# Optimization experiments

Hardware: AMD Instinct MI355X
Metric: run time of the kernel (lower is better)

Reference implementation:

```python
import jax, jax.numpy as jnp
import numpy as np

B, T, S, D, K = 512, 49, 200, 512, 128


def setup_inputs() -> dict:
    key = jax.random.key(0)
    ks = jax.random.split(key, 8)
    return {
        "ifeature": jax.random.normal(ks[0], (B, T, D), dtype=jnp.float32),
        "tfeature_h": jax.random.normal(ks[1], (B, S, D), dtype=jnp.float32),
        "w_Dense_Vi_0": jax.random.normal(ks[2], (D, K), dtype=jnp.float32) * 0.05,
        "w_Dense_Vt_0": jax.random.normal(ks[3], (D, K), dtype=jnp.float32) * 0.05,
        "w_Dense_Pi_0": jax.random.normal(ks[4], (2 * K, 1), dtype=jnp.float32) * 0.05,
        "b_Dense_Pi_0": jnp.zeros((T,), dtype=jnp.float32),
        "w_Dense_Vi_1": jax.random.normal(ks[5], (D, K), dtype=jnp.float32) * 0.05,
        "w_Dense_Vt_1": jax.random.normal(ks[6], (D, K), dtype=jnp.float32) * 0.05,
        "w_Dense_Pi_1": jax.random.normal(ks[7], (2 * K, 1), dtype=jnp.float32) * 0.05,
        "b_Dense_Pi_1": jnp.zeros((S,), dtype=jnp.float32),
    }


def reference(ifeature, tfeature_h, w_Dense_Vi_0, w_Dense_Vt_0, w_Dense_Pi_0,
              b_Dense_Pi_0, w_Dense_Vi_1, w_Dense_Vt_1, w_Dense_Pi_1, b_Dense_Pi_1):
    # tfeature: mean-pooled text, [B, D]
    tfeature = jnp.mean(tfeature_h, axis=1)

    # --- attention over image regions (title_len) ---
    w_Vi_0 = jnp.einsum('btd,dk->btk', ifeature, w_Dense_Vi_0)          # [B,T,K]
    w_Vt_0 = (tfeature @ w_Dense_Vt_0)[:, None, :]                      # [B,1,K] broadcast to T
    Hi = jnp.tanh(jnp.concatenate(
        [w_Vi_0, jnp.broadcast_to(w_Vt_0, w_Vi_0.shape)], axis=-1))     # [B,T,2K]
    Hi_w_b = jnp.einsum('btk,k->bt', Hi, w_Dense_Pi_0[:, 0]) + b_Dense_Pi_0
    Pi = jax.nn.softmax(Hi_w_b, axis=-1)                                # [B,T]
    Vi = jnp.einsum('bt,btd->bd', Pi, ifeature)                         # attended image feature

    # --- attention over text tokens (seq_len) ---
    w_Vi_1 = (Vi @ w_Dense_Vi_1)[:, None, :]                            # [B,1,K]
    w_Vt_1 = jnp.einsum('bsd,dk->bsk', tfeature_h, w_Dense_Vt_1)        # [B,S,K]
    Ht = jnp.tanh(jnp.concatenate(
        [jnp.broadcast_to(w_Vi_1, w_Vt_1.shape), w_Vt_1], axis=-1))     # [B,S,2K]
    Ht_b = jnp.einsum('bsk,k->bs', Ht, w_Dense_Pi_1[:, 0]) + b_Dense_Pi_1
    Pt = jax.nn.softmax(Ht_b, axis=-1)                                  # [B,S]

    # NOTE: original call() returns Pt_Vt (weighted tokens), not the pooled Vt.
    Pt_Vt = Pt[:, :, None] * tfeature_h                                 # [B,S,D]
    return Pt_Vt
```

## Files before the change

### kernel.cpp

```cpp
#include <hip/hip_runtime.h>
#include <math.h>

#define BB 512
#define SS 200
#define DD 512
#define KK 128

typedef __attribute__((ext_vector_type(8))) short bf16x8;
typedef __attribute__((ext_vector_type(4))) float f32x4;

__device__ inline unsigned short f2bf(float f) {
    union { float f; unsigned int u; } v; v.f = f;
    unsigned int r = v.u + 0x7FFFu + ((v.u >> 16) & 1u);
    return (unsigned short)(r >> 16);
}

__global__ void wt_kernel(const float* __restrict__ W, unsigned short* __restrict__ Wt) {
    int i = blockIdx.x * 256 + threadIdx.x;
    int col = i >> 9, d = i & 511;
    Wt[i] = f2bf(W[d * KK + col]);
}

__global__ __launch_bounds__(512, 4) void fused_kernel(
    const float* __restrict__ tfh,
    const unsigned short* __restrict__ Wt,
    const float* __restrict__ wpk,
    const float* __restrict__ bias,
    float* __restrict__ out)
{
    __shared__ unsigned short As[256][40];
    __shared__ unsigned short Bs[128][40];
    __shared__ float logit_s[256];
    __shared__ float Pt[SS];
    __shared__ float wpart[8];

    int tid = threadIdx.x;
    int w   = tid >> 6;
    int l   = tid & 63;
    int l15 = l & 15;
    int g   = l >> 4;
    int b   = blockIdx.x;
    const float* Ab = tfh + (size_t)b * SS * DD;

    f32x4 acc[2][8];
    #pragma unroll
    for (int m = 0; m < 2; ++m)
        #pragma unroll
        for (int n = 0; n < 8; ++n) acc[m][n] = (f32x4){0.f, 0.f, 0.f, 0.f};

    float wv[8];
    #pragma unroll
    for (int n = 0; n < 8; ++n) wv[n] = wpk[n * 16 + l15];

    int ar  = tid >> 1;
    int arc = (ar < SS) ? ar : (SS - 1);
    int ac  = (tid & 1) * 16;
    const float* aptr = Ab + (size_t)arc * DD + ac;
    const unsigned short* bptr = Wt + (size_t)(tid >> 1) * DD + ac;

    for (int d0 = 0; d0 < DD; d0 += 32) {
        {
            const float* s_ = aptr + d0;
            float4 v0 = *(const float4*)(s_);
            float4 v1 = *(const float4*)(s_ + 4);
            float4 v2 = *(const float4*)(s_ + 8);
            float4 v3 = *(const float4*)(s_ + 12);
            bf16x8 p0, p1;
            p0[0] = (short)f2bf(v0.x); p0[1] = (short)f2bf(v0.y);
            p0[2] = (short)f2bf(v0.z); p0[3] = (short)f2bf(v0.w);
            p0[4] = (short)f2bf(v1.x); p0[5] = (short)f2bf(v1.y);
            p0[6] = (short)f2bf(v1.z); p0[7] = (short)f2bf(v1.w);
            p1[0] = (short)f2bf(v2.x); p1[1] = (short)f2bf(v2.y);
            p1[2] = (short)f2bf(v2.z); p1[3] = (short)f2bf(v2.w);
            p1[4] = (short)f2bf(v3.x); p1[5] = (short)f2bf(v3.y);
            p1[6] = (short)f2bf(v3.z); p1[7] = (short)f2bf(v3.w);
            *(bf16x8*)&As[ar][ac]     = p0;
            *(bf16x8*)&As[ar][ac + 8] = p1;
        }
        if (tid < 256) {
            bf16x8 q0 = *(const bf16x8*)(bptr + d0);
            bf16x8 q1 = *(const bf16x8*)(bptr + d0 + 8);
            *(bf16x8*)&Bs[tid >> 1][ac]     = q0;
            *(bf16x8*)&Bs[tid >> 1][ac + 8] = q1;
        }
        __syncthreads();
        bf16x8 af0 = *(const bf16x8*)&As[w * 32 + l15][g * 8];
        bf16x8 af1 = *(const bf16x8*)&As[w * 32 + 16 + l15][g * 8];
        #pragma unroll
        for (int n = 0; n < 8; ++n) {
            bf16x8 bf = *(const bf16x8*)&Bs[n * 16 + l15][g * 8];
            acc[0][n] = __builtin_amdgcn_mfma_f32_16x16x32_bf16(af0, bf, acc[0][n], 0, 0, 0);
            acc[1][n] = __builtin_amdgcn_mfma_f32_16x16x32_bf16(af1, bf, acc[1][n], 0, 0, 0);
        }
        __syncthreads();
    }

    float rs[2][4];
    #pragma unroll
    for (int m = 0; m < 2; ++m)
        #pragma unroll
        for (int r = 0; r < 4; ++r) rs[m][r] = 0.f;
    #pragma unroll
    for (int m = 0; m < 2; ++m)
        #pragma unroll
        for (int n = 0; n < 8; ++n)
            #pragma unroll
            for (int r = 0; r < 4; ++r)
                rs[m][r] += tanhf(acc[m][n][r]) * wv[n];
    #pragma unroll
    for (int m = 0; m < 2; ++m)
        #pragma unroll
        for (int r = 0; r < 4; ++r) {
            float v = rs[m][r];
            v += __shfl_xor(v, 1, 64);
            v += __shfl_xor(v, 2, 64);
            v += __shfl_xor(v, 4, 64);
            v += __shfl_xor(v, 8, 64);
            rs[m][r] = v;
        }
    if (l15 == 0) {
        #pragma unroll
        for (int m = 0; m < 2; ++m)
            #pragma unroll
            for (int r = 0; r < 4; ++r) {
                int srow = w * 32 + m * 16 + g * 4 + r;
                if (srow < SS) logit_s[srow] = rs[m][r] + bias[srow];
            }
    }
    __syncthreads();

    float v = (tid < SS) ? logit_s[tid] : -INFINITY;
    float m = v;
    #pragma unroll
    for (int off = 32; off > 0; off >>= 1) m = fmaxf(m, __shfl_xor(m, off, 64));
    if (l == 0) wpart[w] = m;
    __syncthreads();
    m = -INFINITY;
    #pragma unroll
    for (int i = 0; i < 8; ++i) m = fmaxf(m, wpart[i]);
    float e = (tid < SS) ? expf(v - m) : 0.f;
    float ssum = e;
    #pragma unroll
    for (int off = 32; off > 0; off >>= 1) ssum += __shfl_xor(ssum, off, 64);
    __syncthreads();
    if (l == 0) wpart[w] = ssum;
    __syncthreads();
    ssum = 0.f;
    #pragma unroll
    for (int i = 0; i < 8; ++i) ssum += wpart[i];
    if (tid < SS) Pt[tid] = e / ssum;
    __syncthreads();

    const float4* src = (const float4*)Ab;
    float4*       dst = (float4*)(out + (size_t)b * SS * DD);
    const int n4 = SS * DD / 4;
    for (int i = tid; i < n4; i += 512) {
        float p = Pt[i >> 7];
        float4 x = src[i];
        x.x *= p; x.y *= p; x.z *= p; x.w *= p;
        dst[i] = x;
    }
}

extern "C" void kernel_launch(void* const* d_in, const int* in_sizes, int n_in,
                              void* d_out, int out_size, void* d_ws, size_t ws_size,
                              hipStream_t stream) {
    const float* tfh   = (const float*)d_in[1];
    const float* wVt1  = (const float*)d_in[7];
    const float* wp1   = (const float*)d_in[8];
    const float* bias1 = (const float*)d_in[9];
    float* out = (float*)d_out;

    unsigned short* Wt = (unsigned short*)d_ws;

    wt_kernel<<<KK * DD / 256, 256, 0, stream>>>(wVt1, Wt);
    fused_kernel<<<BB, 512, 0, stream>>>(tfh, Wt, wp1 + KK, bias1, out);
}
```

Baseline: 135.3 us.

## Load A fragments directly into registers and double-buffer B tile with prefetch

Each lane now loads the A-operand fp32 values for its MFMA fragment straight from global memory and converts them to bf16 in registers, so the A shared-memory tile and its store/load round trip are gone. The B tile is double-buffered in LDS, and the next iteration's A and B data are prefetched into registers while the current MFMAs run, leaving one barrier per iteration instead of two. The cost is higher register pressure from the prefetch registers under launch bounds of 512 threads with 4 blocks. Global A loads are also less coalesced, since each lane reads 32 bytes from a different row.

```diff
diff --git a/kernel.cpp b/kernel.cpp
--- a/kernel.cpp
+++ b/kernel.cpp
@@ -15,6 +15,15 @@
     return (unsigned short)(r >> 16);
 }
 
+__device__ inline bf16x8 pack8(const float4& a, const float4& b) {
+    bf16x8 p;
+    p[0] = (short)f2bf(a.x); p[1] = (short)f2bf(a.y);
+    p[2] = (short)f2bf(a.z); p[3] = (short)f2bf(a.w);
+    p[4] = (short)f2bf(b.x); p[5] = (short)f2bf(b.y);
+    p[6] = (short)f2bf(b.z); p[7] = (short)f2bf(b.w);
+    return p;
+}
+
 __global__ void wt_kernel(const float* __restrict__ W, unsigned short* __restrict__ Wt) {
     int i = blockIdx.x * 256 + threadIdx.x;
     int col = i >> 9, d = i & 511;
@@ -28,8 +37,7 @@
     const float* __restrict__ bias,
     float* __restrict__ out)
 {
-    __shared__ unsigned short As[256][40];
-    __shared__ unsigned short Bs[128][40];
+    __shared__ unsigned short Bs[2][KK][40];
     __shared__ float logit_s[256];
     __shared__ float Pt[SS];
     __shared__ float wpart[8];
@@ -42,6 +50,16 @@
     int b   = blockIdx.x;
     const float* Ab = tfh + (size_t)b * SS * DD;
 
+    int row0 = w * 32 + l15;
+    int row1 = row0 + 16;
+    bool v0 = row0 < SS, v1 = row1 < SS;
+    const float* a0 = Ab + (size_t)row0 * DD + g * 8;
+    const float* a1 = Ab + (size_t)row1 * DD + g * 8;
+
+    int brow = tid >> 2;
+    int bcol = (tid & 3) * 8;
+    const unsigned short* bp = Wt + (size_t)brow * DD + bcol;
+
     f32x4 acc[2][8];
     #pragma unroll
     for (int m = 0; m < 2; ++m)
@@ -52,47 +70,39 @@
     #pragma unroll
     for (int n = 0; n < 8; ++n) wv[n] = wpk[n * 16 + l15];
 
-    int ar  = tid >> 1;
-    int arc = (ar < SS) ? ar : (SS - 1);
-    int ac  = (tid & 1) * 16;
-    const float* aptr = Ab + (size_t)arc * DD + ac;
-    const unsigned short* bptr = Wt + (size_t)(tid >> 1) * DD + ac;
+    const float4 fz = make_float4(0.f, 0.f, 0.f, 0.f);
 
-    for (int d0 = 0; d0 < DD; d0 += 32) {
-        {
-            const float* s_ = aptr + d0;
-            float4 v0 = *(const float4*)(s_);
-            float4 v1 = *(const float4*)(s_ + 4);
-            float4 v2 = *(const float4*)(s_ + 8);
-            float4 v3 = *(const float4*)(s_ + 12);
-            bf16x8 p0, p1;
-            p0[0] = (short)f2bf(v0.x); p0[1] = (short)f2bf(v0.y);
-            p0[2] = (short)f2bf(v0.z); p0[3] = (short)f2bf(v0.w);
-            p0[4] = (short)f2bf(v1.x); p0[5] = (short)f2bf(v1.y);
-            p0[6] = (short)f2bf(v1.z); p0[7] = (short)f2bf(v1.w);
-            p1[0] = (short)f2bf(v2.x); p1[1] = (short)f2bf(v2.y);
-            p1[2] = (short)f2bf(v2.z); p1[3] = (short)f2bf(v2.w);
-            p1[4] = (short)f2bf(v3.x); p1[5] = (short)f2bf(v3.y);
-            p1[6] = (short)f2bf(v3.z); p1[7] = (short)f2bf(v3.w);
-            *(bf16x8*)&As[ar][ac]     = p0;
-            *(bf16x8*)&As[ar][ac + 8] = p1;
+    float4 cA00 = v0 ? *(const float4*)(a0)     : fz;
+    float4 cA01 = v0 ? *(const float4*)(a0 + 4) : fz;
+    float4 cA10 = v1 ? *(const float4*)(a1)     : fz;
+    float4 cA11 = v1 ? *(const float4*)(a1 + 4) : fz;
+    *(bf16x8*)&Bs[0][brow][bcol] = *(const bf16x8*)(bp);
+    __syncthreads();
+
+    #pragma unroll 2
+    for (int t = 0; t < 16; ++t) {
+        int p = t & 1;
+        float4 nA00, nA01, nA10, nA11;
+        bf16x8 nB;
+        if (t < 15) {
+            int d = (t + 1) * 32;
+            nA00 = v0 ? *(const float4*)(a0 + d)     : fz;
+            nA01 = v0 ? *(const float4*)(a0 + d + 4) : fz;
+            nA10 = v1 ? *(const float4*)(a1 + d)     : fz;
+            nA11 = v1 ? *(const float4*)(a1 + d + 4) : fz;
+            nB   = *(const bf16x8*)(bp + d);
         }
-        if (tid < 256) {
-            bf16x8 q0 = *(const bf16x8*)(bptr + d0);
-            bf16x8 q1 = *(const bf16x8*)(bptr + d0 + 8);
-            *(bf16x8*)&Bs[tid >> 1][ac]     = q0;
-            *(bf16x8*)&Bs[tid >> 1][ac + 8] = q1;
-        }
-        __syncthreads();
-        bf16x8 af0 = *(const bf16x8*)&As[w * 32 + l15][g * 8];
-        bf16x8 af1 = *(const bf16x8*)&As[w * 32 + 16 + l15][g * 8];
+        bf16x8 af0 = pack8(cA00, cA01);
+        bf16x8 af1 = pack8(cA10, cA11);
         #pragma unroll
         for (int n = 0; n < 8; ++n) {
-            bf16x8 bf = *(const bf16x8*)&Bs[n * 16 + l15][g * 8];
-            acc[0][n] = __builtin_amdgcn_mfma_f32_16x16x32_bf16(af0, bf, acc[0][n], 0, 0, 0);
-            acc[1][n] = __builtin_amdgcn_mfma_f32_16x16x32_bf16(af1, bf, acc[1][n], 0, 0, 0);
+            bf16x8 bfv = *(const bf16x8*)&Bs[p][n * 16 + l15][g * 8];
+            acc[0][n] = __builtin_amdgcn_mfma_f32_16x16x32_bf16(af0, bfv, acc[0][n], 0, 0, 0);
+            acc[1][n] = __builtin_amdgcn_mfma_f32_16x16x32_bf16(af1, bfv, acc[1][n], 0, 0, 0);
         }
+        if (t < 15) *(bf16x8*)&Bs[p ^ 1][brow][bcol] = nB;
         __syncthreads();
+        cA00 = nA00; cA01 = nA01; cA10 = nA10; cA11 = nA11;
     }
 
     float rs[2][4];
```

Measured after the change: 141.1 us. 4.3% more time.
